# Performance work log

Measured on AMD Instinct MI355X. Metric: run time of the kernel, lower is better.

The kernel has to match this reference:

```python
import jax, jax.numpy as jnp
import numpy as np

B, C_IN, C_MID, HW, EMB, N_ATTR = 512, 1024, 512, 14, 1024, 8
BN_EPS = 1e-5


def setup_inputs() -> dict:
    key = jax.random.key(0)
    ks = jax.random.split(key, 20)
    s = lambda *sh: 1.0 / np.sqrt(sh[-1])
    return {
        "x": jax.random.normal(ks[0], (B, C_IN, HW, HW), jnp.float32),
        "c": jax.random.randint(ks[1], (B,), 0, N_ATTR),
        "attr_emb": jax.random.normal(ks[2], (N_ATTR, 512), jnp.float32),
        "Wt1": jax.random.normal(ks[3], (512, 512), jnp.float32) * s(512, 512),
        "bt1": jnp.zeros((512,), jnp.float32),
        "Wc": jax.random.normal(ks[4], (C_MID, C_IN), jnp.float32) * s(C_MID, C_IN),
        "bc": jnp.zeros((C_MID,), jnp.float32),
        "bn_gamma": jnp.ones((C_MID,), jnp.float32),
        "bn_beta": jnp.zeros((C_MID,), jnp.float32),
        "bn_mean": jnp.zeros((C_MID,), jnp.float32),
        "bn_var": jax.random.uniform(ks[5], (C_MID,), jnp.float32, 0.5, 1.5),
        "Wt2": jax.random.normal(ks[6], (512, 512), jnp.float32) * s(512, 512),
        "bt2": jnp.zeros((512,), jnp.float32),
        "W1": jax.random.normal(ks[7], (512, 1536), jnp.float32) * s(512, 1536),
        "b1": jnp.zeros((512,), jnp.float32),
        "W2": jax.random.normal(ks[8], (1024, 512), jnp.float32) * s(1024, 512),
        "b2": jnp.zeros((1024,), jnp.float32),
        "Wf": jax.random.normal(ks[9], (EMB, 1024), jnp.float32) * s(EMB, 1024),
        "bf": jnp.zeros((EMB,), jnp.float32),
    }


def reference(x, c, attr_emb, Wt1, bt1, Wc, bc, bn_gamma, bn_beta, bn_mean, bn_var,
              Wt2, bt2, W1, b1, W2, b2, Wf, bf):
    # conv1 (1x1) + BN (inference stats) + tanh -> img: [B, 512, 14, 14]
    img = jnp.einsum('bchw,oc->bohw', x, Wc) + bc[None, :, None, None]
    inv_std = jax.lax.rsqrt(bn_var + BN_EPS)
    img = (img - bn_mean[None, :, None, None]) * (bn_gamma * inv_std)[None, :, None, None] \
          + bn_beta[None, :, None, None]
    img = jnp.tanh(img)
    # attribute query: [B, 512]
    emb = attr_emb[c]
    attr = jnp.tanh(emb @ Wt1.T + bt1)
    # attention map: channel dot product, scale, spatial softmax
    attmap = jnp.einsum('bk,bkhw->bhw', attr, img) / np.sqrt(512.0)  # [B,14,14]
    attmap = jax.nn.softmax(attmap.reshape(B, -1), axis=-1).reshape(B, HW, HW)
    # attended feature: [B, 1024]
    feat = jnp.einsum('bchw,bhw->bc', x, attmap)
    # gated fusion
    attr2 = jax.nn.relu(emb @ Wt2.T + bt2)
    img_attr = jnp.concatenate([feat, attr2], axis=1)  # [B, 1536]
    mask = jax.nn.sigmoid(jax.nn.relu(img_attr @ W1.T + b1) @ W2.T + b2)
    out = (feat * mask) @ Wf.T + bf  # [B, EMB]
    # l2norm over dim 1
    norm = jnp.sqrt(jnp.sum(out * out, axis=1, keepdims=True))
    return out / norm
```

## Files before the change

### kernel.cpp

```cpp
#include <hip/hip_runtime.h>
#include <math.h>

#define HW2 196
#define CIN 1024

using f32x4 = __attribute__((ext_vector_type(4))) float;
using s16x8 = __attribute__((ext_vector_type(8))) short;

__device__ __forceinline__ unsigned int f2bfu(float f) {
  union { float f; unsigned int i; } v; v.f = f;
  unsigned int r = v.i + 0x7FFFu + ((v.i >> 16) & 1u);
  return r >> 16;
}
__device__ __forceinline__ float tanh_fast(float x) {
  float cx = fminf(fmaxf(x, -15.f), 15.f);
  float e = __expf(2.f * cx);
  return (e - 1.f) / (e + 1.f);
}

__global__ void k_pre1(const float* __restrict__ attr_emb,
                       const float* __restrict__ Wt1, const float* __restrict__ bt1,
                       const float* __restrict__ Wt2, const float* __restrict__ bt2,
                       const float* __restrict__ bc, const float* __restrict__ gamma,
                       const float* __restrict__ beta, const float* __restrict__ mean,
                       const float* __restrict__ var,
                       float* __restrict__ attr1_tab, float* __restrict__ attr2_tab,
                       float* __restrict__ bnA, float* __restrict__ bnB) {
  int gid = blockIdx.x * 256 + threadIdx.x;
  if (gid < 4096) {
    int a = gid >> 9, j = gid & 511;
    const float* e = attr_emb + a * 512;
    const float* w1 = Wt1 + j * 512;
    const float* w2 = Wt2 + j * 512;
    float d1 = 0.f, d2 = 0.f;
    for (int i = 0; i < 512; ++i) {
      float ev = e[i];
      d1 += ev * w1[i];
      d2 += ev * w2[i];
    }
    attr1_tab[gid] = tanh_fast(d1 + bt1[j]);
    float r = d2 + bt2[j];
    attr2_tab[gid] = r > 0.f ? r : 0.f;
  } else if (gid < 4608) {
    int o = gid - 4096;
    float A = gamma[o] * rsqrtf(var[o] + 1e-5f);
    bnA[o] = A;
    bnB[o] = (bc[o] - mean[o]) * A + beta[o];
  }
}

__global__ void k_pre2(const float* __restrict__ W1, const float* __restrict__ b1,
                       const float* __restrict__ attr2_tab, float* __restrict__ t2) {
  int gid = blockIdx.x * 256 + threadIdx.x;
  int a = gid >> 9, j = gid & 511;
  const float* w = W1 + (size_t)j * 1536 + 1024;
  const float* at = attr2_tab + a * 512;
  float d = 0.f;
  for (int i = 0; i < 512; ++i) d += w[i] * at[i];
  t2[gid] = d + b1[j];
}

__global__ __launch_bounds__(256, 2) void k_main(
    const float* __restrict__ x, const float* __restrict__ Wc,
    const int* __restrict__ cidx, const float* __restrict__ attr1_tab,
    const float* __restrict__ bnA, const float* __restrict__ bnB,
    float* __restrict__ feat) {
  __shared__ __align__(16) unsigned short Xc[32 * 210];
  __shared__ __align__(16) unsigned short Wl[128 * 40];
  __shared__ float attr_l[512], bnA_l[512], bnB_l[512];
  __shared__ float s_lds[HW2];
  __shared__ float red[8];

  int b = blockIdx.x, tid = threadIdx.x;
  int wid = tid >> 6, lane = tid & 63, quad = lane >> 4, l15 = lane & 15;

  int ca = cidx[b];
  for (int i = tid; i < 512; i += 256) {
    attr_l[i] = attr1_tab[ca * 512 + i];
    bnA_l[i] = bnA[i];
    bnB_l[i] = bnB[i];
  }
  if (tid < 224) {
    int row = tid / 7, i = tid - row * 7;
    *(unsigned int*)&Xc[row * 210 + 196 + 2 * i] = 0u;
  }

  const float* xb = x + (size_t)b * (CIN * HW2);
  int t0 = wid * 3;
  int ntile = (wid == 3) ? 4 : 3;

  float sv[4][4];
#pragma unroll
  for (int mt = 0; mt < 4; ++mt)
#pragma unroll
    for (int r = 0; r < 4; ++r) sv[mt][r] = 0.f;

  for (int och = 0; och < 4; ++och) {
    int o_base = och * 128;
    f32x4 acc[4][8];
#pragma unroll
    for (int mt = 0; mt < 4; ++mt)
#pragma unroll
      for (int q = 0; q < 8; ++q) {
        f32x4 z = {0.f, 0.f, 0.f, 0.f};
        acc[mt][q] = z;
      }
    for (int kt = 0; kt < 32; ++kt) {
      __syncthreads();
      int c0 = kt * 32;
      const float* xs = xb + (size_t)c0 * HW2;
#pragma unroll
      for (int it = 0; it < 7; ++it) {
        int idx = it * 256 + tid;
        if (idx < 1568) {
          int row = idx / 49, col = idx - row * 49;
          f32x4 v = *(const f32x4*)(xs + idx * 4);
          unsigned int* tp = (unsigned int*)&Xc[row * 210 + col * 4];
          tp[0] = f2bfu(v.x) | (f2bfu(v.y) << 16);
          tp[1] = f2bfu(v.z) | (f2bfu(v.w) << 16);
        }
      }
#pragma unroll
      for (int r = 0; r < 2; ++r) {
        int ch = r * 256 + tid;
        int orow = ch >> 2, part = ch & 3;
        const float* wr = Wc + (size_t)(o_base + orow) * CIN + c0 + part * 8;
        f32x4 va = *(const f32x4*)wr;
        f32x4 vb = *(const f32x4*)(wr + 4);
        unsigned int* tp = (unsigned int*)&Wl[orow * 40 + part * 8];
        tp[0] = f2bfu(va.x) | (f2bfu(va.y) << 16);
        tp[1] = f2bfu(va.z) | (f2bfu(va.w) << 16);
        tp[2] = f2bfu(vb.x) | (f2bfu(vb.y) << 16);
        tp[3] = f2bfu(vb.z) | (f2bfu(vb.w) << 16);
      }
      __syncthreads();
      s16x8 af[4];
#pragma unroll
      for (int mt = 0; mt < 4; ++mt)
        if (mt < ntile) {
          int hw = (t0 + mt) * 16 + l15;
#pragma unroll
          for (int j = 0; j < 8; ++j)
            af[mt][j] = (short)Xc[(quad * 8 + j) * 210 + hw];
        }
#pragma unroll
      for (int h = 0; h < 2; ++h) {
        s16x8 bfr[4];
#pragma unroll
        for (int nt = 0; nt < 4; ++nt)
          bfr[nt] = *(const s16x8*)&Wl[(h * 64 + nt * 16 + l15) * 40 + quad * 8];
#pragma unroll
        for (int mt = 0; mt < 4; ++mt)
          if (mt < ntile) {
#pragma unroll
            for (int nt = 0; nt < 4; ++nt)
              acc[mt][h * 4 + nt] = __builtin_amdgcn_mfma_f32_16x16x32_bf16(
                  af[mt], bfr[nt], acc[mt][h * 4 + nt], 0, 0, 0);
          }
      }
    }
    float at[8], sa[8], sb[8];
#pragma unroll
    for (int q = 0; q < 8; ++q) {
      int o = o_base + q * 16 + l15;
      at[q] = attr_l[o]; sa[q] = bnA_l[o]; sb[q] = bnB_l[o];
    }
#pragma unroll
    for (int mt = 0; mt < 4; ++mt)
      if (mt < ntile) {
#pragma unroll
        for (int r = 0; r < 4; ++r) {
          float v = 0.f;
#pragma unroll
          for (int q = 0; q < 8; ++q)
            v += at[q] * tanh_fast(acc[mt][q][r] * sa[q] + sb[q]);
          sv[mt][r] += v;
        }
      }
  }
#pragma unroll
  for (int mt = 0; mt < 4; ++mt)
    if (mt < ntile) {
#pragma unroll
      for (int r = 0; r < 4; ++r) {
        float v = sv[mt][r];
        v += __shfl_xor(v, 1);
        v += __shfl_xor(v, 2);
        v += __shfl_xor(v, 4);
        v += __shfl_xor(v, 8);
        int hw = (t0 + mt) * 16 + quad * 4 + r;
        if (l15 == 0 && hw < HW2) s_lds[hw] = v;
      }
    }
  __syncthreads();
  {
    float v = (tid < HW2) ? s_lds[tid] * 0.04419417382415922f : -1e30f;
    float m = v;
    for (int off = 32; off > 0; off >>= 1) m = fmaxf(m, __shfl_xor(m, off));
    if (lane == 0) red[wid] = m;
    __syncthreads();
    float gm = fmaxf(fmaxf(red[0], red[1]), fmaxf(red[2], red[3]));
    float e = (tid < HW2) ? __expf(v - gm) : 0.f;
    float s = e;
    for (int off = 32; off > 0; off >>= 1) s += __shfl_xor(s, off);
    __syncthreads();
    if (lane == 0) red[wid] = s;
    __syncthreads();
    float gs = red[0] + red[1] + red[2] + red[3];
    if (tid < HW2) s_lds[tid] = e / gs;
  }
  __syncthreads();
  for (int cc = tid; cc < 1024; cc += 256) {
    const float* xr = xb + (size_t)cc * HW2;
    float a = 0.f;
#pragma unroll
    for (int h4 = 0; h4 < 49; ++h4) {
      f32x4 v = *(const f32x4*)(xr + h4 * 4);
      a += s_lds[h4 * 4 + 0] * v.x + s_lds[h4 * 4 + 1] * v.y +
           s_lds[h4 * 4 + 2] * v.z + s_lds[h4 * 4 + 3] * v.w;
    }
    feat[(size_t)b * 1024 + cc] = a;
  }
}

__device__ __forceinline__ void dot8(const float* __restrict__ w,
                                     const float* __restrict__ fa, const float* __restrict__ fb,
                                     int i, float& a0, float& a1) {
  f32x4 wa = *(const f32x4*)(w + i);
  f32x4 wb = *(const f32x4*)(w + i + 4);
  a0 += wa.x * fa[i+0]; a1 += wa.x * fb[i+0];
  a0 += wa.y * fa[i+1]; a1 += wa.y * fb[i+1];
  a0 += wa.z * fa[i+2]; a1 += wa.z * fb[i+2];
  a0 += wa.w * fa[i+3]; a1 += wa.w * fb[i+3];
  a0 += wb.x * fa[i+4]; a1 += wb.x * fb[i+4];
  a0 += wb.y * fa[i+5]; a1 += wb.y * fb[i+5];
  a0 += wb.z * fa[i+6]; a1 += wb.z * fb[i+6];
  a0 += wb.w * fa[i+7]; a1 += wb.w * fb[i+7];
}

__global__ __launch_bounds__(512) void k_mlp(
    const float* __restrict__ feat, const int* __restrict__ cidx, const float* __restrict__ t2,
    const float* __restrict__ W1, const float* __restrict__ W2,
    const float* __restrict__ b2, const float* __restrict__ Wf,
    const float* __restrict__ bfb, float* __restrict__ out) {
  __shared__ float f0[1024], f1[1024];
  __shared__ float h0[512], h1[512];
  __shared__ float g0[1024], g1[1024];
  __shared__ float red[16];
  int tid = threadIdx.x;
  int b0 = blockIdx.x * 2, b1 = b0 + 1;
  int c0 = cidx[b0], c1 = cidx[b1];
  for (int i = tid; i < 1024; i += 512) {
    f0[i] = feat[(size_t)b0 * 1024 + i];
    f1[i] = feat[(size_t)b1 * 1024 + i];
  }
  __syncthreads();
  {
    int j = tid;
    const float* w = W1 + (size_t)j * 1536;
    float a0 = 0.f, a1 = 0.f;
    for (int i = 0; i < 1024; i += 8) dot8(w, f0, f1, i, a0, a1);
    h0[j] = fmaxf(a0 + t2[c0 * 512 + j], 0.f);
    h1[j] = fmaxf(a1 + t2[c1 * 512 + j], 0.f);
  }
  __syncthreads();
  for (int m = tid; m < 1024; m += 512) {
    const float* w = W2 + (size_t)m * 512;
    float a0 = 0.f, a1 = 0.f;
    for (int i = 0; i < 512; i += 8) dot8(w, h0, h1, i, a0, a1);
    float bb = b2[m];
    float s0 = 1.f / (1.f + __expf(-(a0 + bb)));
    float s1 = 1.f / (1.f + __expf(-(a1 + bb)));
    g0[m] = f0[m] * s0;
    g1[m] = f1[m] * s1;
  }
  __syncthreads();
  float o0[2], o1[2];
  float ss0 = 0.f, ss1 = 0.f;
#pragma unroll
  for (int t = 0; t < 2; ++t) {
    int e = tid + t * 512;
    const float* w = Wf + (size_t)e * 1024;
    float a0 = 0.f, a1 = 0.f;
    for (int i = 0; i < 1024; i += 8) dot8(w, g0, g1, i, a0, a1);
    float bb = bfb[e];
    a0 += bb; a1 += bb;
    o0[t] = a0; o1[t] = a1;
    ss0 += a0 * a0; ss1 += a1 * a1;
  }
  for (int off = 32; off > 0; off >>= 1) {
    ss0 += __shfl_xor(ss0, off);
    ss1 += __shfl_xor(ss1, off);
  }
  int wid = tid >> 6, lane = tid & 63;
  if (lane == 0) { red[wid] = ss0; red[wid + 8] = ss1; }
  __syncthreads();
  float t0 = 0.f, t1 = 0.f;
#pragma unroll
  for (int w = 0; w < 8; ++w) { t0 += red[w]; t1 += red[w + 8]; }
  float n0 = rsqrtf(t0), n1 = rsqrtf(t1);
#pragma unroll
  for (int t = 0; t < 2; ++t) {
    int e = tid + t * 512;
    out[(size_t)b0 * 1024 + e] = o0[t] * n0;
    out[(size_t)b1 * 1024 + e] = o1[t] * n1;
  }
}

extern "C" void kernel_launch(void* const* d_in, const int* in_sizes, int n_in,
                              void* d_out, int out_size, void* d_ws, size_t ws_size,
                              hipStream_t stream) {
  const float* x        = (const float*)d_in[0];
  const int*   c        = (const int*)d_in[1];
  const float* attr_emb = (const float*)d_in[2];
  const float* Wt1      = (const float*)d_in[3];
  const float* bt1      = (const float*)d_in[4];
  const float* Wc       = (const float*)d_in[5];
  const float* bc       = (const float*)d_in[6];
  const float* gamma    = (const float*)d_in[7];
  const float* beta     = (const float*)d_in[8];
  const float* mean     = (const float*)d_in[9];
  const float* var      = (const float*)d_in[10];
  const float* Wt2      = (const float*)d_in[11];
  const float* bt2      = (const float*)d_in[12];
  const float* W1       = (const float*)d_in[13];
  const float* b1       = (const float*)d_in[14];
  const float* W2       = (const float*)d_in[15];
  const float* b2       = (const float*)d_in[16];
  const float* Wf       = (const float*)d_in[17];
  const float* bfb      = (const float*)d_in[18];

  char* ws = (char*)d_ws;
  float* feat      = (float*)ws;
  float* attr1_tab = (float*)(ws + 2097152);
  float* attr2_tab = attr1_tab + 4096;
  float* t2        = attr2_tab + 4096;
  float* bnA       = t2 + 4096;
  float* bnB       = bnA + 512;

  hipLaunchKernelGGL(k_pre1, dim3(18), dim3(256), 0, stream,
                     attr_emb, Wt1, bt1, Wt2, bt2, bc, gamma, beta, mean, var,
                     attr1_tab, attr2_tab, bnA, bnB);
  hipLaunchKernelGGL(k_pre2, dim3(16), dim3(256), 0, stream, W1, b1, attr2_tab, t2);
  hipLaunchKernelGGL(k_main, dim3(512), dim3(256), 0, stream,
                     x, Wc, c, attr1_tab, bnA, bnB, feat);
  hipLaunchKernelGGL(k_mlp, dim3(256), dim3(512), 0, stream,
                     feat, c, t2, W1, W2, b2, Wf, bfb, (float*)d_out);
}
```

Baseline: 1.422 ms.

## Pre-convert Wc to bf16, transpose X tile with swizzle, widen K step

Wc is converted to bf16 once, in an extra part of the k_pre2 launch, so k_main loads bf16 weights directly instead of converting fp32 per block per tile. The X tile is now stored transposed (hw-major) in LDS with an XOR swizzle, which lets A fragments be read as one 16-byte vector instead of eight scalar short loads. The K step is doubled to 64 channels, halving the number of barrier pairs. LDS use grows, which may reduce occupancy, and the transposed X stores are 8-byte scattered writes.

```diff
diff --git a/kernel.cpp b/kernel.cpp
--- a/kernel.cpp
+++ b/kernel.cpp
@@ -1,4 +1,5 @@
 #include <hip/hip_runtime.h>
+#include <hip/hip_bf16.h>
 #include <math.h>
 
 #define HW2 196
@@ -7,15 +8,16 @@
 using f32x4 = __attribute__((ext_vector_type(4))) float;
 using s16x8 = __attribute__((ext_vector_type(8))) short;
 
-__device__ __forceinline__ unsigned int f2bfu(float f) {
-  union { float f; unsigned int i; } v; v.f = f;
-  unsigned int r = v.i + 0x7FFFu + ((v.i >> 16) & 1u);
-  return r >> 16;
-}
 __device__ __forceinline__ float tanh_fast(float x) {
   float cx = fminf(fmaxf(x, -15.f), 15.f);
   float e = __expf(2.f * cx);
   return (e - 1.f) / (e + 1.f);
+}
+
+__device__ __forceinline__ unsigned int pkbf(float a, float b) {
+  union { __hip_bfloat162 h; unsigned int u; } v;
+  v.h = __float22bfloat162_rn(make_float2(a, b));
+  return v.u;
 }
 
 __global__ void k_pre1(const float* __restrict__ attr_emb,
@@ -50,23 +52,39 @@
 }
 
 __global__ void k_pre2(const float* __restrict__ W1, const float* __restrict__ b1,
-                       const float* __restrict__ attr2_tab, float* __restrict__ t2) {
-  int gid = blockIdx.x * 256 + threadIdx.x;
-  int a = gid >> 9, j = gid & 511;
-  const float* w = W1 + (size_t)j * 1536 + 1024;
-  const float* at = attr2_tab + a * 512;
-  float d = 0.f;
-  for (int i = 0; i < 512; ++i) d += w[i] * at[i];
-  t2[gid] = d + b1[j];
+                       const float* __restrict__ attr2_tab, float* __restrict__ t2,
+                       const float* __restrict__ Wc, unsigned short* __restrict__ wcbf) {
+  int bid = blockIdx.x;
+  if (bid < 16) {
+    int gid = bid * 256 + threadIdx.x;
+    int a = gid >> 9, j = gid & 511;
+    const float* w = W1 + (size_t)j * 1536 + 1024;
+    const float* at = attr2_tab + a * 512;
+    float d = 0.f;
+    for (int i = 0; i < 512; ++i) d += w[i] * at[i];
+    t2[gid] = d + b1[j];
+  } else {
+    int idx = (bid - 16) * 256 + threadIdx.x;
+    const float* src = Wc + (size_t)idx * 16;
+    f32x4 a0 = *(const f32x4*)src;
+    f32x4 a1 = *(const f32x4*)(src + 4);
+    f32x4 a2 = *(const f32x4*)(src + 8);
+    f32x4 a3 = *(const f32x4*)(src + 12);
+    unsigned int* dp = (unsigned int*)&wcbf[(size_t)idx * 16];
+    dp[0] = pkbf(a0.x, a0.y); dp[1] = pkbf(a0.z, a0.w);
+    dp[2] = pkbf(a1.x, a1.y); dp[3] = pkbf(a1.z, a1.w);
+    dp[4] = pkbf(a2.x, a2.y); dp[5] = pkbf(a2.z, a2.w);
+    dp[6] = pkbf(a3.x, a3.y); dp[7] = pkbf(a3.z, a3.w);
+  }
 }
 
 __global__ __launch_bounds__(256, 2) void k_main(
-    const float* __restrict__ x, const float* __restrict__ Wc,
+    const float* __restrict__ x, const unsigned short* __restrict__ wcbf,
     const int* __restrict__ cidx, const float* __restrict__ attr1_tab,
     const float* __restrict__ bnA, const float* __restrict__ bnB,
     float* __restrict__ feat) {
-  __shared__ __align__(16) unsigned short Xc[32 * 210];
-  __shared__ __align__(16) unsigned short Wl[128 * 40];
+  __shared__ __align__(16) unsigned short Xt[208 * 72];
+  __shared__ __align__(16) unsigned short Wl[128 * 72];
   __shared__ float attr_l[512], bnA_l[512], bnB_l[512];
   __shared__ float s_lds[HW2];
   __shared__ float red[8];
@@ -80,9 +98,9 @@
     bnA_l[i] = bnA[i];
     bnB_l[i] = bnB[i];
   }
-  if (tid < 224) {
-    int row = tid / 7, i = tid - row * 7;
-    *(unsigned int*)&Xc[row * 210 + 196 + 2 * i] = 0u;
+  {
+    unsigned int* zp = (unsigned int*)&Xt[196 * 72];
+    for (int i = tid; i < 432; i += 256) zp[i] = 0u;
   }
 
   const float* xb = x + (size_t)b * (CIN * HW2);
@@ -105,58 +123,66 @@
         f32x4 z = {0.f, 0.f, 0.f, 0.f};
         acc[mt][q] = z;
       }
-    for (int kt = 0; kt < 32; ++kt) {
+    for (int kt = 0; kt < 16; ++kt) {
       __syncthreads();
-      int c0 = kt * 32;
+      int c0 = kt * 64;
       const float* xs = xb + (size_t)c0 * HW2;
 #pragma unroll
-      for (int it = 0; it < 7; ++it) {
-        int idx = it * 256 + tid;
-        if (idx < 1568) {
-          int row = idx / 49, col = idx - row * 49;
-          f32x4 v = *(const f32x4*)(xs + idx * 4);
-          unsigned int* tp = (unsigned int*)&Xc[row * 210 + col * 4];
-          tp[0] = f2bfu(v.x) | (f2bfu(v.y) << 16);
-          tp[1] = f2bfu(v.z) | (f2bfu(v.w) << 16);
+      for (int it = 0; it < 4; ++it) {
+        int id = it * 256 + tid;
+        if (id < 784) {
+          int cq = id / 49;
+          int hw4 = id - cq * 49;
+          const float* p = xs + (size_t)cq * (4 * HW2) + hw4 * 4;
+          f32x4 v0 = *(const f32x4*)p;
+          f32x4 v1 = *(const f32x4*)(p + HW2);
+          f32x4 v2 = *(const f32x4*)(p + 2 * HW2);
+          f32x4 v3 = *(const f32x4*)(p + 3 * HW2);
+          int s = (hw4 & 7) << 1;
+          int ub = (cq ^ s) << 2;
+#pragma unroll
+          for (int r = 0; r < 4; ++r) {
+            unsigned long long wv =
+                (unsigned long long)pkbf(v0[r], v1[r]) |
+                ((unsigned long long)pkbf(v2[r], v3[r]) << 32);
+            *(unsigned long long*)&Xt[(hw4 * 4 + r) * 72 + ub] = wv;
+          }
         }
       }
 #pragma unroll
-      for (int r = 0; r < 2; ++r) {
-        int ch = r * 256 + tid;
-        int orow = ch >> 2, part = ch & 3;
-        const float* wr = Wc + (size_t)(o_base + orow) * CIN + c0 + part * 8;
-        f32x4 va = *(const f32x4*)wr;
-        f32x4 vb = *(const f32x4*)(wr + 4);
-        unsigned int* tp = (unsigned int*)&Wl[orow * 40 + part * 8];
-        tp[0] = f2bfu(va.x) | (f2bfu(va.y) << 16);
-        tp[1] = f2bfu(va.z) | (f2bfu(va.w) << 16);
-        tp[2] = f2bfu(vb.x) | (f2bfu(vb.y) << 16);
-        tp[3] = f2bfu(vb.z) | (f2bfu(vb.w) << 16);
+      for (int it = 0; it < 4; ++it) {
+        int ch = it * 256 + tid;
+        int row = ch >> 3, u = ch & 7;
+        s16x8 v = *(const s16x8*)&wcbf[(size_t)(o_base + row) * CIN + c0 + u * 8];
+        *(s16x8*)&Wl[row * 72 + u * 8] = v;
       }
       __syncthreads();
-      s16x8 af[4];
-#pragma unroll
-      for (int mt = 0; mt < 4; ++mt)
-        if (mt < ntile) {
-          int hw = (t0 + mt) * 16 + l15;
-#pragma unroll
-          for (int j = 0; j < 8; ++j)
-            af[mt][j] = (short)Xc[(quad * 8 + j) * 210 + hw];
-        }
-#pragma unroll
-      for (int h = 0; h < 2; ++h) {
-        s16x8 bfr[4];
-#pragma unroll
-        for (int nt = 0; nt < 4; ++nt)
-          bfr[nt] = *(const s16x8*)&Wl[(h * 64 + nt * 16 + l15) * 40 + quad * 8];
+#pragma unroll
+      for (int kk = 0; kk < 2; ++kk) {
+        s16x8 af[4];
 #pragma unroll
         for (int mt = 0; mt < 4; ++mt)
           if (mt < ntile) {
-#pragma unroll
-            for (int nt = 0; nt < 4; ++nt)
-              acc[mt][h * 4 + nt] = __builtin_amdgcn_mfma_f32_16x16x32_bf16(
-                  af[mt], bfr[nt], acc[mt][h * 4 + nt], 0, 0, 0);
+            int hw = (t0 + mt) * 16 + l15;
+            int s = ((hw >> 2) & 7) << 1;
+            int u = (kk << 3) + (quad << 1);
+            af[mt] = *(const s16x8*)&Xt[hw * 72 + ((u ^ s) << 2)];
           }
+#pragma unroll
+        for (int h = 0; h < 2; ++h) {
+          s16x8 bfr[4];
+#pragma unroll
+          for (int nt = 0; nt < 4; ++nt)
+            bfr[nt] = *(const s16x8*)&Wl[(h * 64 + nt * 16 + l15) * 72 + kk * 32 + quad * 8];
+#pragma unroll
+          for (int mt = 0; mt < 4; ++mt)
+            if (mt < ntile) {
+#pragma unroll
+              for (int nt = 0; nt < 4; ++nt)
+                acc[mt][h * 4 + nt] = __builtin_amdgcn_mfma_f32_16x16x32_bf16(
+                    af[mt], bfr[nt], acc[mt][h * 4 + nt], 0, 0, 0);
+            }
+        }
       }
     }
     float at[8], sa[8], sb[8];
@@ -337,13 +363,15 @@
   float* t2        = attr2_tab + 4096;
   float* bnA       = t2 + 4096;
   float* bnB       = bnA + 512;
+  unsigned short* wcbf = (unsigned short*)(ws + 2150400);
 
   hipLaunchKernelGGL(k_pre1, dim3(18), dim3(256), 0, stream,
                      attr_emb, Wt1, bt1, Wt2, bt2, bc, gamma, beta, mean, var,
                      attr1_tab, attr2_tab, bnA, bnB);
-  hipLaunchKernelGGL(k_pre2, dim3(16), dim3(256), 0, stream, W1, b1, attr2_tab, t2);
+  hipLaunchKernelGGL(k_pre2, dim3(144), dim3(256), 0, stream,
+                     W1, b1, attr2_tab, t2, Wc, wcbf);
   hipLaunchKernelGGL(k_main, dim3(512), dim3(256), 0, stream,
-                     x, Wc, c, attr1_tab, bnA, bnB, feat);
+                     x, wcbf, c, attr1_tab, bnA, bnB, feat);
   hipLaunchKernelGGL(k_mlp, dim3(256), dim3(512), 0, stream,
                      feat, c, t2, W1, W2, b2, Wf, bfb, (float*)d_out);
 }
```

New measurement: 1.217 ms. -14.4%, faster.
